# Kernel tuning notes

Hardware: AMD Instinct MI355X
Metric: run time of the kernel (lower is better)

Reference implementation:

```python
import jax, jax.numpy as jnp
import numpy as np

N_NODES = 100000
N_EDGES = 1600000
D_FEAT = 64


def setup_inputs() -> dict:
    key = jax.random.key(0)
    k1, k2, k3, k4 = jax.random.split(key, 4)
    rows = jnp.sort(jax.random.randint(k1, (N_EDGES,), 0, N_NODES, dtype=jnp.int64))
    cols = jax.random.randint(k2, (N_EDGES,), 0, N_NODES, dtype=jnp.int64)
    vals = jax.random.uniform(k3, (N_EDGES,), dtype=jnp.float32)
    embeds = jax.random.normal(k4, (N_NODES, D_FEAT), dtype=jnp.float32)
    return {"rows": rows, "cols": cols, "vals": vals, "embeds": embeds}


def reference(rows, cols, vals, embeds):
    # out[i] = sum_{e: rows[e]==i} vals[e] * embeds[cols[e]]  (torch.spmm with COO adj)
    gathered = vals[:, None] * embeds[cols]          # [E, d]
    out = jax.ops.segment_sum(gathered, rows, num_segments=N_NODES)  # [N, d]
    return out
```

## Files before the change

kernel.cpp:

```cpp
#include <hip/hip_runtime.h>
#include <hip/hip_bf16.h>


constexpr int D = 64;

__device__ __forceinline__ unsigned bf16rnd(unsigned u) {
    return (u + 0x7FFFu + ((u >> 16) & 1u)) >> 16;
}

__global__ __launch_bounds__(256) void prep_kernel(
    const uint4* __restrict__ src,
    uint4* __restrict__ dst,
    int n8,
    const int* __restrict__ rows, int* __restrict__ row_ptr,
    int n_edges, int n_nodes, int cvt_blocks)
{
    if ((int)blockIdx.x < cvt_blocks) {
        int i = blockIdx.x * 256 + threadIdx.x;
        if (i >= n8) return;
        uint4 a = src[2 * i];
        uint4 b = src[2 * i + 1];
        uint4 o;
        o.x = bf16rnd(a.x) | (bf16rnd(a.y) << 16);
        o.y = bf16rnd(a.z) | (bf16rnd(a.w) << 16);
        o.z = bf16rnd(b.x) | (bf16rnd(b.y) << 16);
        o.w = bf16rnd(b.z) | (bf16rnd(b.w) << 16);
        dst[i] = o;
    } else {
        int e = (blockIdx.x - cvt_blocks) * 256 + threadIdx.x;
        if (e >= n_edges) return;
        int r_cur  = rows[e];
        int r_prev = (e == 0) ? -1 : rows[e - 1];
        for (int r = r_prev + 1; r <= r_cur; ++r) row_ptr[r] = e;
        if (e == n_edges - 1)
            for (int r = r_cur + 1; r <= n_nodes; ++r) row_ptr[r] = n_edges;
    }
}

__device__ __forceinline__ float bflo(unsigned w) {
    union { unsigned u; float f; } x; x.u = w << 16; return x.f;
}
__device__ __forceinline__ float bfhi(unsigned w) {
    union { unsigned u; float f; } x; x.u = w & 0xFFFF0000u; return x.f;
}

__global__ __launch_bounds__(256) void spmm_node_kernel(
    const int* __restrict__ row_ptr,
    const int* __restrict__ cols,
    const float* __restrict__ vals,
    const uint4* __restrict__ ebf4,
    float4* __restrict__ out4,
    int n_nodes)
{
    const int lane = threadIdx.x & 63;
    const int t    = lane & 7;
    const int s    = lane >> 3;
    const int wave = blockIdx.x * (blockDim.x >> 6) + (threadIdx.x >> 6);
    const int node = wave * 8 + s;
    if (node >= n_nodes) return;

    const int lo = row_ptr[node];
    const int hi = row_ptr[node + 1];

    float4 acc0 = make_float4(0.f, 0.f, 0.f, 0.f);
    float4 acc1 = make_float4(0.f, 0.f, 0.f, 0.f);

    for (int e = lo; e < hi; e += 4) {
        const int last = hi - 1;
        int i0 = e;
        int i1 = (e + 1 <= last) ? e + 1 : last;
        int i2 = (e + 2 <= last) ? e + 2 : last;
        int i3 = (e + 3 <= last) ? e + 3 : last;

        int c0 = cols[i0], c1 = cols[i1], c2 = cols[i2], c3 = cols[i3];

        float v0 = vals[i0];
        float v1 = (e + 1 < hi) ? vals[i1] : 0.f;
        float v2 = (e + 2 < hi) ? vals[i2] : 0.f;
        float v3 = (e + 3 < hi) ? vals[i3] : 0.f;

        uint4 m0 = ebf4[c0 * 8 + t];
        uint4 m1 = ebf4[c1 * 8 + t];
        uint4 m2 = ebf4[c2 * 8 + t];
        uint4 m3 = ebf4[c3 * 8 + t];

        acc0.x += v0 * bflo(m0.x); acc0.y += v0 * bfhi(m0.x);
        acc0.z += v0 * bflo(m0.y); acc0.w += v0 * bfhi(m0.y);
        acc1.x += v0 * bflo(m0.z); acc1.y += v0 * bfhi(m0.z);
        acc1.z += v0 * bflo(m0.w); acc1.w += v0 * bfhi(m0.w);

        acc0.x += v1 * bflo(m1.x); acc0.y += v1 * bfhi(m1.x);
        acc0.z += v1 * bflo(m1.y); acc0.w += v1 * bfhi(m1.y);
        acc1.x += v1 * bflo(m1.z); acc1.y += v1 * bfhi(m1.z);
        acc1.z += v1 * bflo(m1.w); acc1.w += v1 * bfhi(m1.w);

        acc0.x += v2 * bflo(m2.x); acc0.y += v2 * bfhi(m2.x);
        acc0.z += v2 * bflo(m2.y); acc0.w += v2 * bfhi(m2.y);
        acc1.x += v2 * bflo(m2.z); acc1.y += v2 * bfhi(m2.z);
        acc1.z += v2 * bflo(m2.w); acc1.w += v2 * bfhi(m2.w);

        acc0.x += v3 * bflo(m3.x); acc0.y += v3 * bfhi(m3.x);
        acc0.z += v3 * bflo(m3.y); acc0.w += v3 * bfhi(m3.y);
        acc1.x += v3 * bflo(m3.z); acc1.y += v3 * bfhi(m3.z);
        acc1.z += v3 * bflo(m3.w); acc1.w += v3 * bfhi(m3.w);
    }

    long ob = (long)node * 16 + 2 * t;
    out4[ob]     = acc0;
    out4[ob + 1] = acc1;
}

extern "C" void kernel_launch(void* const* d_in, const int* in_sizes, int n_in,
                              void* d_out, int out_size, void* d_ws, size_t ws_size,
                              hipStream_t stream) {
    const int*   rows   = (const int*)d_in[0];
    const int*   cols   = (const int*)d_in[1];
    const float* vals   = (const float*)d_in[2];
    const float* embeds = (const float*)d_in[3];
    float4*      out4   = (float4*)d_out;

    const int n_edges = in_sizes[0];
    const int n_nodes = out_size / D;
    const int n_feat  = in_sizes[3];

    char*  ws        = (char*)d_ws;
    uint4* ebf_table = (uint4*)ws;
    int*   row_ptr   = (int*)(ws + (size_t)n_feat * 2);

    int n8         = n_feat / 8;
    int cvt_blocks = (n8 + 255) / 256;
    int row_blocks = (n_edges + 255) / 256;
    prep_kernel<<<cvt_blocks + row_blocks, 256, 0, stream>>>(
        (const uint4*)embeds, ebf_table, n8,
        rows, row_ptr, n_edges, n_nodes, cvt_blocks);

    int waves  = (n_nodes + 7) / 8;
    int blocks = (waves + 3) / 4;
    spmm_node_kernel<<<blocks, 256, 0, stream>>>(
        row_ptr, cols, vals, ebf_table, out4, n_nodes);
}
```

Before: 124.2 us.

## Stage each wave's edge cols/vals into LDS with coalesced loads before gathering

Each wave now loads the contiguous cols and vals range covering its eight nodes into per-wave shared memory in chunks of 256, using coalesced 64-lane loads. The gather loop then reads column indices and weights from LDS instead of issuing scattered per-node global loads. This targets uncoalesced index and value traffic, at the cost of an extra LDS round-trip, wave barriers, and 8 KB of shared memory per block, which may reduce occupancy.

```diff
diff --git a/kernel.cpp b/kernel.cpp
--- a/kernel.cpp
+++ b/kernel.cpp
@@ -52,57 +52,85 @@
     float4* __restrict__ out4,
     int n_nodes)
 {
+    constexpr int CHUNK = 256;
+    __shared__ int   s_cols[4][CHUNK];
+    __shared__ float s_vals[4][CHUNK];
+
     const int lane = threadIdx.x & 63;
     const int t    = lane & 7;
     const int s    = lane >> 3;
-    const int wave = blockIdx.x * (blockDim.x >> 6) + (threadIdx.x >> 6);
+    const int w    = threadIdx.x >> 6;
+    const int wave = blockIdx.x * (blockDim.x >> 6) + w;
     const int node = wave * 8 + s;
     if (node >= n_nodes) return;
 
-    const int lo = row_ptr[node];
-    const int hi = row_ptr[node + 1];
+    const int nb    = wave * 8;
+    const int nbhi  = (nb + 8 <= n_nodes) ? nb + 8 : n_nodes;
+    const int wbase = row_ptr[nb];
+    const int wend  = row_ptr[nbhi];
+    const int lo    = row_ptr[node];
+    const int hi    = row_ptr[node + 1];
 
     float4 acc0 = make_float4(0.f, 0.f, 0.f, 0.f);
     float4 acc1 = make_float4(0.f, 0.f, 0.f, 0.f);
 
-    for (int e = lo; e < hi; e += 4) {
-        const int last = hi - 1;
-        int i0 = e;
-        int i1 = (e + 1 <= last) ? e + 1 : last;
-        int i2 = (e + 2 <= last) ? e + 2 : last;
-        int i3 = (e + 3 <= last) ? e + 3 : last;
+    for (int cbase = wbase; cbase < wend; cbase += CHUNK) {
+        #pragma unroll
+        for (int j = 0; j < CHUNK; j += 64) {
+            if (cbase + j >= wend) break;
+            int idx = cbase + j + lane;
+            if (idx < wend) {
+                s_cols[w][j + lane] = cols[idx];
+                s_vals[w][j + lane] = vals[idx];
+            }
+        }
+        __builtin_amdgcn_wave_barrier();
 
-        int c0 = cols[i0], c1 = cols[i1], c2 = cols[i2], c3 = cols[i3];
+        const int cend = (cbase + CHUNK < wend) ? cbase + CHUNK : wend;
+        int e0 = (lo > cbase) ? lo : cbase;
+        int e1 = (hi < cend)  ? hi : cend;
 
-        float v0 = vals[i0];
-        float v1 = (e + 1 < hi) ? vals[i1] : 0.f;
-        float v2 = (e + 2 < hi) ? vals[i2] : 0.f;
-        float v3 = (e + 3 < hi) ? vals[i3] : 0.f;
+        for (int e = e0; e < e1; e += 4) {
+            const int last = e1 - 1;
+            int i0 = e - cbase;
+            int i1 = ((e + 1 <= last) ? e + 1 : last) - cbase;
+            int i2 = ((e + 2 <= last) ? e + 2 : last) - cbase;
+            int i3 = ((e + 3 <= last) ? e + 3 : last) - cbase;
 
-        uint4 m0 = ebf4[c0 * 8 + t];
-        uint4 m1 = ebf4[c1 * 8 + t];
-        uint4 m2 = ebf4[c2 * 8 + t];
-        uint4 m3 = ebf4[c3 * 8 + t];
+            int c0 = s_cols[w][i0], c1 = s_cols[w][i1];
+            int c2 = s_cols[w][i2], c3 = s_cols[w][i3];
 
-        acc0.x += v0 * bflo(m0.x); acc0.y += v0 * bfhi(m0.x);
-        acc0.z += v0 * bflo(m0.y); acc0.w += v0 * bfhi(m0.y);
-        acc1.x += v0 * bflo(m0.z); acc1.y += v0 * bfhi(m0.z);
-        acc1.z += v0 * bflo(m0.w); acc1.w += v0 * bfhi(m0.w);
+            float v0 = s_vals[w][i0];
+            float v1 = (e + 1 < e1) ? s_vals[w][i1] : 0.f;
+            float v2 = (e + 2 < e1) ? s_vals[w][i2] : 0.f;
+            float v3 = (e + 3 < e1) ? s_vals[w][i3] : 0.f;
 
-        acc0.x += v1 * bflo(m1.x); acc0.y += v1 * bfhi(m1.x);
-        acc0.z += v1 * bflo(m1.y); acc0.w += v1 * bfhi(m1.y);
-        acc1.x += v1 * bflo(m1.z); acc1.y += v1 * bfhi(m1.z);
-        acc1.z += v1 * bflo(m1.w); acc1.w += v1 * bfhi(m1.w);
+            uint4 m0 = ebf4[c0 * 8 + t];
+            uint4 m1 = ebf4[c1 * 8 + t];
+            uint4 m2 = ebf4[c2 * 8 + t];
+            uint4 m3 = ebf4[c3 * 8 + t];
 
-        acc0.x += v2 * bflo(m2.x); acc0.y += v2 * bfhi(m2.x);
-        acc0.z += v2 * bflo(m2.y); acc0.w += v2 * bfhi(m2.y);
-        acc1.x += v2 * bflo(m2.z); acc1.y += v2 * bfhi(m2.z);
-        acc1.z += v2 * bflo(m2.w); acc1.w += v2 * bfhi(m2.w);
+            acc0.x += v0 * bflo(m0.x); acc0.y += v0 * bfhi(m0.x);
+            acc0.z += v0 * bflo(m0.y); acc0.w += v0 * bfhi(m0.y);
+            acc1.x += v0 * bflo(m0.z); acc1.y += v0 * bfhi(m0.z);
+            acc1.z += v0 * bflo(m0.w); acc1.w += v0 * bfhi(m0.w);
 
-        acc0.x += v3 * bflo(m3.x); acc0.y += v3 * bfhi(m3.x);
-        acc0.z += v3 * bflo(m3.y); acc0.w += v3 * bfhi(m3.y);
-        acc1.x += v3 * bflo(m3.z); acc1.y += v3 * bfhi(m3.z);
-        acc1.z += v3 * bflo(m3.w); acc1.w += v3 * bfhi(m3.w);
+            acc0.x += v1 * bflo(m1.x); acc0.y += v1 * bfhi(m1.x);
+            acc0.z += v1 * bflo(m1.y); acc0.w += v1 * bfhi(m1.y);
+            acc1.x += v1 * bflo(m1.z); acc1.y += v1 * bfhi(m1.z);
+            acc1.z += v1 * bflo(m1.w); acc1.w += v1 * bfhi(m1.w);
+
+            acc0.x += v2 * bflo(m2.x); acc0.y += v2 * bfhi(m2.x);
+            acc0.z += v2 * bflo(m2.y); acc0.w += v2 * bfhi(m2.y);
+            acc1.x += v2 * bflo(m2.z); acc1.y += v2 * bfhi(m2.z);
+            acc1.z += v2 * bflo(m2.w); acc1.w += v2 * bfhi(m2.w);
+
+            acc0.x += v3 * bflo(m3.x); acc0.y += v3 * bfhi(m3.x);
+            acc0.z += v3 * bflo(m3.y); acc0.w += v3 * bfhi(m3.y);
+            acc1.x += v3 * bflo(m3.z); acc1.y += v3 * bfhi(m3.z);
+            acc1.z += v3 * bflo(m3.w); acc1.w += v3 * bfhi(m3.w);
+        }
+        __builtin_amdgcn_wave_barrier();
     }
 
     long ob = (long)node * 16 + 2 * t;
```

Measured after the change: 120.6 us. -2.8%, faster.
